# Optimization experiments

Measured on AMD Instinct MI355X. Metric: run time of the kernel, lower is better.

The kernel has to match this reference:

```python
import jax, jax.numpy as jnp
import numpy as np

FRACTION = 0.33  # from attn_type='query_selector_0.33'


def setup_inputs() -> dict:
    key = jax.random.key(0)
    k1, k2, k3, k4 = jax.random.split(key, 4)
    B, L, DIM_VAL, DIM_ATTN = 8, 4096, 64, 64
    scale = 1.0 / np.sqrt(DIM_VAL).astype(np.float32)
    x = jax.random.normal(k1, (B, L, DIM_VAL), dtype=jnp.float32)
    Wq = jax.random.normal(k2, (DIM_VAL, DIM_ATTN), dtype=jnp.float32) * scale
    Wk = jax.random.normal(k3, (DIM_VAL, DIM_ATTN), dtype=jnp.float32) * scale
    Wv = jax.random.normal(k4, (DIM_VAL, DIM_VAL), dtype=jnp.float32) * scale
    return {"x": x, "Wq": Wq, "Wk": Wk, "Wv": Wv}


def reference(x, Wq, Wk, Wv):
    # Projections (bias-free Linears)
    Q = jnp.einsum('bld,de->ble', x, Wq)  # [B, L, Da]
    K = jnp.einsum('bld,de->ble', x, Wk)  # [B, L, Da]
    V = jnp.einsum('bld,de->ble', x, Wv)  # [B, L, Dv]

    B, L_Q, Da = Q.shape
    l_Q = int((1.0 - FRACTION) * L_Q)  # static: shapes known at trace time

    # keys.topk(l_Q, dim=1).values -> per-channel top-l_Q along seq; mean over them
    K_top = jax.lax.top_k(jnp.swapaxes(K, 1, 2), l_Q)[0]  # [B, Da, l_Q]
    K_reduce = K_top.mean(axis=-1)                         # [B, Da]

    # score each query against the reduced key; pick top-l_Q queries
    sqk = jnp.einsum('bd,bld->bl', K_reduce, Q)            # [B, L_Q]
    indices = jax.lax.top_k(sqk, l_Q)[1]                   # [B, l_Q] int32

    # gather sampled queries
    Q_sample = jnp.take_along_axis(Q, indices[:, :, None], axis=1)  # [B, l_Q, Da]

    # dense attention for the sampled queries only
    scores = jnp.einsum('bqd,bkd->bqk', Q_sample, K) / jnp.sqrt(jnp.asarray(Da, Q.dtype))
    attn = jax.nn.softmax(scores, axis=-1)                 # [B, l_Q, L]
    out_sel = jnp.einsum('bqk,bkv->bqv', attn, V)          # [B, l_Q, Dv]

    # mean-filled result, scatter attention outputs to selected rows
    mean_values = V.mean(axis=-2)                          # [B, Dv]
    result = jnp.broadcast_to(mean_values[:, None, :], (B, L_Q, V.shape[-1]))
    result = result.at[jnp.arange(B)[:, None], indices].set(out_sel)
    return result
```

## Files before the change

### kernel.cpp

```cpp
#include <hip/hip_runtime.h>
#include <hip/hip_bf16.h>
#include <math.h>

#define BATCH 8
#define SEQ   4096
#define DIM   64
#define LQ    2744
#define QPB   128
#define NQB   22
#define QPAD  2816
#define KS    8
#define L2E   1.4426950408889634f
#define QSC   0.1803368801111204f

typedef _Float16 half8 __attribute__((ext_vector_type(8)));
typedef short    bs8   __attribute__((ext_vector_type(8)));
typedef float    fx16  __attribute__((ext_vector_type(16)));
typedef unsigned short ushort_t;

union UH { uint4 u4; half8 h; };
union UB { unsigned u[4]; uint4 u4; bs8 s; };

__device__ __forceinline__ unsigned pack_bf16(float a, float b) {
    unsigned ua = __float_as_uint(a), ub = __float_as_uint(b);
    ua += 0x7FFFu + ((ua >> 16) & 1u);
    ub += 0x7FFFu + ((ub >> 16) & 1u);
    return (ua >> 16) | (ub & 0xFFFF0000u);
}

__device__ __forceinline__ unsigned f2sort(float f) {
    unsigned u = __float_as_uint(f);
    return (u & 0x80000000u) ? ~u : (u | 0x80000000u);
}
__device__ __forceinline__ float sort2f(unsigned u) {
    return __uint_as_float((u & 0x80000000u) ? (u & 0x7FFFFFFFu) : ~u);
}

template <int NT>
__device__ void radix_select_4096(const unsigned* u, int k, unsigned* hist,
                                  unsigned* scan, unsigned* res) {
    const int t = threadIdx.x;
    if (t == 0) { res[0] = 0u; res[1] = (unsigned)k; }
    for (int pass = 3; pass >= 0; --pass) {
        const int shift = pass * 8;
        if (t < 256) hist[t] = 0u;
        __syncthreads();
        const unsigned pref  = res[0];
        const unsigned kk    = res[1];
        const unsigned hmask = (pass == 3) ? 0u : (0xFFFFFFFFu << (shift + 8));
        for (int i = t; i < 4096; i += NT) {
            unsigned ui = u[i];
            if ((ui & hmask) == pref) atomicAdd(&hist[(ui >> shift) & 255u], 1u);
        }
        __syncthreads();
        unsigned h = 0u, s = 0u;
        if (t < 256) { h = hist[t]; s = h; scan[t] = s; }
        __syncthreads();
#pragma unroll
        for (int ofs = 1; ofs < 256; ofs <<= 1) {
            unsigned add = (t < 256 && t + ofs < 256) ? scan[t + ofs] : 0u;
            __syncthreads();
            if (t < 256) { s += add; scan[t] = s; }
            __syncthreads();
        }
        if (t < 256 && s >= kk && (s - h) < kk) {
            res[0] = pref | ((unsigned)t << shift);
            res[1] = kk - (s - h);
        }
        __syncthreads();
    }
}

__global__ __launch_bounds__(256) void proj_kernel(
    const float* __restrict__ x,  const float* __restrict__ Wq,
    const float* __restrict__ Wk, const float* __restrict__ Wv,
    float* __restrict__ Q, float* __restrict__ Kt,
    _Float16* __restrict__ Qh, _Float16* __restrict__ Kh,
    ushort_t* __restrict__ Vt, float* __restrict__ pmean) {
    const int rt = blockIdx.x, b = blockIdx.y, t = threadIdx.x;
    __shared__ float4 xs4[64 * 17];
    __shared__ float  red[4][64];
    {
        const float4* xg = (const float4*)(x + ((size_t)b * SEQ + rt * 64) * DIM);
        for (int i = 0; i < 4; ++i) {
            int s = t + 256 * i;
            xs4[(s >> 4) * 17 + (s & 15)] = xg[s];
        }
    }
    __syncthreads();
    const int ch = t & 63, rg = t >> 6;
    float accq[16], acck[16], accv[16];
#pragma unroll
    for (int i = 0; i < 16; ++i) { accq[i] = 0.f; acck[i] = 0.f; accv[i] = 0.f; }
    for (int dc = 0; dc < 4; ++dc) {
        float wq[16], wk[16], wv[16];
#pragma unroll
        for (int dd = 0; dd < 16; ++dd) {
            int d = dc * 16 + dd;
            wq[dd] = Wq[d * 64 + ch]; wk[dd] = Wk[d * 64 + ch]; wv[dd] = Wv[d * 64 + ch];
        }
        for (int r = 0; r < 16; ++r) {
            const int row = rg * 16 + r;
            const float4* xr = &xs4[row * 17 + dc * 4];
            float xv[16];
            float4 a0 = xr[0], a1 = xr[1], a2 = xr[2], a3 = xr[3];
            xv[0]=a0.x; xv[1]=a0.y; xv[2]=a0.z; xv[3]=a0.w;
            xv[4]=a1.x; xv[5]=a1.y; xv[6]=a1.z; xv[7]=a1.w;
            xv[8]=a2.x; xv[9]=a2.y; xv[10]=a2.z; xv[11]=a2.w;
            xv[12]=a3.x; xv[13]=a3.y; xv[14]=a3.z; xv[15]=a3.w;
#pragma unroll
            for (int dd = 0; dd < 16; ++dd) {
                accq[r] = fmaf(xv[dd], wq[dd], accq[r]);
                acck[r] = fmaf(xv[dd], wk[dd], acck[r]);
                accv[r] = fmaf(xv[dd], wv[dd], accv[r]);
            }
        }
    }
    const int rowbase = rt * 64 + rg * 16;
    float sv = 0.f;
#pragma unroll
    for (int r = 0; r < 16; ++r) {
        size_t o = ((size_t)b * SEQ + rowbase + r) * DIM + ch;
        Q[o]  = accq[r];
        Qh[o] = (_Float16)(accq[r] * QSC);
        Kh[o] = (_Float16)acck[r];
        sv += accv[r];
    }
    float4* ktp = (float4*)(Kt + ((size_t)b * 64 + ch) * SEQ + rowbase);
    ktp[0] = make_float4(acck[0], acck[1], acck[2], acck[3]);
    ktp[1] = make_float4(acck[4], acck[5], acck[6], acck[7]);
    ktp[2] = make_float4(acck[8], acck[9], acck[10], acck[11]);
    ktp[3] = make_float4(acck[12], acck[13], acck[14], acck[15]);
    {
        unsigned pk[8];
#pragma unroll
        for (int i = 0; i < 8; ++i) {
            __hip_bfloat162 h2 = __float22bfloat162_rn(make_float2(accv[2*i], accv[2*i+1]));
            union { __hip_bfloat162 h; unsigned u; } cv; cv.h = h2;
            pk[i] = cv.u;
        }
        uint4* vp = (uint4*)(Vt + ((size_t)(b * 64 + ch)) * SEQ + rowbase);
        vp[0] = make_uint4(pk[0], pk[1], pk[4], pk[5]);
        vp[1] = make_uint4(pk[2], pk[3], pk[6], pk[7]);
    }
    red[rg][ch] = sv;
    __syncthreads();
    if (rg == 0)
        pmean[((size_t)b * 64 + ch) * 64 + rt] =
            red[0][ch] + red[1][ch] + red[2][ch] + red[3][ch];
}

__global__ __launch_bounds__(1024) void kmean_kernel(const float* __restrict__ Kt,
                                                     const float* __restrict__ pmean,
                                                     float* __restrict__ Kred,
                                                     float* __restrict__ meanfin) {
    __shared__ unsigned u[4096];
    __shared__ unsigned hist[256];
    __shared__ unsigned scan[256];
    __shared__ unsigned res[2];
    __shared__ float rsum[16];
    const int bc = blockIdx.x, t = threadIdx.x;
    if (t < 64) {
        float v = pmean[(size_t)bc * 64 + t];
        for (int m = 1; m < 64; m <<= 1) v += __shfl_xor(v, m, 64);
        if (t == 0) meanfin[bc] = v * (1.0f / (float)SEQ);
    }
    const float4* c4 = (const float4*)(Kt + (size_t)bc * SEQ);
    if (t < 1024) {
        float4 v = c4[t];
        u[t*4+0] = f2sort(v.x); u[t*4+1] = f2sort(v.y);
        u[t*4+2] = f2sort(v.z); u[t*4+3] = f2sort(v.w);
    }
    __syncthreads();
    radix_select_4096<1024>(u, LQ, hist, scan, res);
    const unsigned Tu = res[0];
    const int krem = (int)res[1];
    float loc = 0.f;
    for (int i = t; i < 4096; i += 1024)
        if (u[i] > Tu) loc += sort2f(u[i]);
    for (int msk = 1; msk < 64; msk <<= 1) loc += __shfl_xor(loc, msk, 64);
    if ((t & 63) == 0) rsum[t >> 6] = loc;
    __syncthreads();
    if (t == 0) {
        float s = (float)krem * sort2f(Tu);
        for (int i = 0; i < 16; ++i) s += rsum[i];
        Kred[bc] = s / (float)LQ;
    }
}

__global__ __launch_bounds__(1024) void select_kernel(const float* __restrict__ Q,
                                                      const float* __restrict__ Kred,
                                                      int* __restrict__ sel,
                                                      int* __restrict__ inv) {
    __shared__ unsigned u[4096];
    __shared__ unsigned hist[256];
    __shared__ unsigned scan[256];
    __shared__ unsigned res[2];
    __shared__ float kr[64];
    __shared__ int eq_idx[256];
    __shared__ int cnts[2];
    const int b = blockIdx.x, t = threadIdx.x;
    if (t < 64) kr[t] = Kred[b * 64 + t];
    if (t < 2) cnts[t] = 0;
    int* invb = inv + (size_t)b * SEQ;
    __syncthreads();
    for (int row = t; row < 4096; row += 1024) {
        const float4* q = (const float4*)(Q + ((size_t)b * SEQ + row) * DIM);
        float s = 0.f;
#pragma unroll
        for (int i = 0; i < 16; ++i) {
            float4 v = q[i];
            s = fmaf(v.x, kr[i*4+0], s); s = fmaf(v.y, kr[i*4+1], s);
            s = fmaf(v.z, kr[i*4+2], s); s = fmaf(v.w, kr[i*4+3], s);
        }
        u[row] = f2sort(s);
        invb[row] = -1;
    }
    __syncthreads();
    radix_select_4096<1024>(u, LQ, hist, scan, res);
    const unsigned Tu = res[0];
    const int krem = (int)res[1];
    int* selb = sel + b * QPAD;
    for (int i = t; i < 4096; i += 1024) {
        unsigned ui = u[i];
        if (ui > Tu) {
            int p = atomicAdd(&cnts[0], 1);
            selb[p] = i;
            invb[i] = p;
        } else if (ui == Tu) {
            int p = atomicAdd(&cnts[1], 1);
            if (p < 256) eq_idx[p] = i;
        }
    }
    __syncthreads();
    if (t == 0) {
        int ng = cnts[0];
        int ne = cnts[1] < 256 ? cnts[1] : 256;
        for (int i = 1; i < ne; ++i) {
            int v = eq_idx[i], j = i - 1;
            while (j >= 0 && eq_idx[j] > v) { eq_idx[j+1] = eq_idx[j]; --j; }
            eq_idx[j+1] = v;
        }
        for (int j = 0; j < krem; ++j) {
            selb[ng + j] = eq_idx[j];
            invb[eq_idx[j]] = ng + j;
        }
    }
    __syncthreads();
    if (t < QPAD - LQ) selb[LQ + t] = selb[LQ - 1];
}

__global__ __launch_bounds__(256, 3) void attn_kernel(
    const ushort_t* __restrict__ Qh, const ushort_t* __restrict__ Kh,
    const ushort_t* __restrict__ Vt, const int* __restrict__ sel,
    float* __restrict__ pl, float* __restrict__ pout) {
    const int qt = blockIdx.x, ks = blockIdx.y, b = blockIdx.z;
    const int t = threadIdx.x, w = t >> 6, lane = t & 63;
    const int col = lane & 31, h = lane >> 5;

    __shared__ ushort_t Ktile[2][32 * 64];
    __shared__ ushort_t Vtile[2][32 * 64];

    half8 qf[4];
    {
        const int q = qt * QPB + w * 32 + col;
        const int row = sel[b * QPAD + q];
        const uint4* qg = (const uint4*)(Qh + ((size_t)b * SEQ + row) * DIM);
#pragma unroll
        for (int m = 0; m < 4; ++m) { UH u; u.u4 = qg[2 * m + h]; qf[m] = u.h; }
    }

    int koff[4], voff[4];
#pragma unroll
    for (int m = 0; m < 4; ++m)
        koff[m] = col * 64 + 8 * ((2 * m + h) ^ (col & 7));
#pragma unroll
    for (int i = 0; i < 4; ++i)
        voff[i] = col * 64 + 8 * ((i * 2 + h) ^ (col & 7));

    fx16 O0, O1;
#pragma unroll
    for (int r = 0; r < 16; ++r) { O0[r] = 0.f; O1[r] = 0.f; }
    float l = 0.f;

    const int srow = t >> 3, sgr = t & 7;
    const int lg = sgr ^ (srow & 7);
    const int vD = lg >> 2, vc = (lg >> 1) & 1, vh = lg & 1;
    const size_t kgbase = ((size_t)b * SEQ + ks * 512 + srow) * DIM + 8 * lg;
    const size_t vgbase = ((size_t)(b * DIM + srow + 32 * vD)) * SEQ
                          + ks * 512 + vc * 16 + vh * 8;

    uint4 kreg = *(const uint4*)(Kh + kgbase);
    uint4 vreg = *(const uint4*)(Vt + vgbase);

    for (int tile = 0; tile < 16; ++tile) {
        const int buf = tile & 1;
        *(uint4*)&Ktile[buf][srow * 64 + sgr * 8] = kreg;
        *(uint4*)&Vtile[buf][srow * 64 + sgr * 8] = vreg;
        __syncthreads();
        if (tile < 15) {
            kreg = *(const uint4*)(Kh + kgbase + (size_t)(tile + 1) * 32 * DIM);
            vreg = *(const uint4*)(Vt + vgbase + (size_t)(tile + 1) * 32);
        }
        fx16 S;
#pragma unroll
        for (int r = 0; r < 16; ++r) S[r] = 0.f;
#pragma unroll
        for (int m = 0; m < 4; ++m) {
            UH kf;
            kf.u4 = *(const uint4*)&Ktile[buf][koff[m]];
            S = __builtin_amdgcn_mfma_f32_32x32x16_f16(kf.h, qf[m], S, 0, 0, 0);
        }
        float p[16];
#pragma unroll
        for (int r = 0; r < 16; ++r) p[r] = __builtin_amdgcn_exp2f(S[r]);
#pragma unroll
        for (int r = 0; r < 16; ++r) l += p[r];
        UB A0, A1;
#pragma unroll
        for (int v = 0; v < 4; ++v) {
            A0.u[v] = pack_bf16(p[2 * v],     p[2 * v + 1]);
            A1.u[v] = pack_bf16(p[8 + 2 * v], p[8 + 2 * v + 1]);
        }
#pragma unroll
        for (int D = 0; D < 2; ++D) {
            fx16& O = D ? O1 : O0;
#pragma unroll
            for (int c = 0; c < 2; ++c) {
                UB vf;
                vf.u4 = *(const uint4*)&Vtile[buf][voff[D * 2 + c]];
                O = __builtin_amdgcn_mfma_f32_32x32x16_bf16(c ? A1.s : A0.s, vf.s, O, 0, 0, 0);
            }
        }
    }

    l += __shfl_xor(l, 32);

    const int qg0 = qt * QPB + w * 32;
    const size_t base = (size_t)b * QPAD + qg0;
#pragma unroll
    for (int D = 0; D < 2; ++D) {
        const fx16& O = D ? O1 : O0;
#pragma unroll
        for (int r = 0; r < 16; ++r) {
            const int q = (r & 3) + 8 * (r >> 2) + 4 * h;
            atomicAdd(&pout[(base + q) * DIM + D * 32 + col], O[r]);
        }
    }
    if (h == 0) atomicAdd(&pl[base + col], l);
}

__global__ __launch_bounds__(256) void comb_kernel(
    const float* __restrict__ pl, const float* __restrict__ pout,
    const int* __restrict__ inv, const float* __restrict__ meanfin,
    float* __restrict__ out) {
    const int idx = blockIdx.x * 256 + threadIdx.x;
    const int b = idx >> 16;
    const int rc = idx & 65535;
    const int row = rc >> 4, c = rc & 15;
    const int p = inv[b * SEQ + row];
    float4 o;
    if (p >= 0) {
        const size_t s0 = (size_t)b * QPAD + p;
        const float invl = 1.0f / pl[s0];
        float4 a = ((const float4*)(pout + s0 * DIM))[c];
        o = make_float4(a.x * invl, a.y * invl, a.z * invl, a.w * invl);
    } else {
        o = make_float4(meanfin[b * 64 + c * 4 + 0], meanfin[b * 64 + c * 4 + 1],
                        meanfin[b * 64 + c * 4 + 2], meanfin[b * 64 + c * 4 + 3]);
    }
    ((float4*)out)[idx] = o;
}

extern "C" void kernel_launch(void* const* d_in, const int* in_sizes, int n_in,
                              void* d_out, int out_size, void* d_ws, size_t ws_size,
                              hipStream_t stream) {
    const float* x  = (const float*)d_in[0];
    const float* Wq = (const float*)d_in[1];
    const float* Wk = (const float*)d_in[2];
    const float* Wv = (const float*)d_in[3];
    float* out = (float*)d_out;
    char* wsb  = (char*)d_ws;

    float*    Q       = (float*)(wsb);
    _Float16* Qh      = (_Float16*)(wsb + 8388608);
    _Float16* Kh      = (_Float16*)(wsb + 12582912);
    ushort_t* Vt      = (ushort_t*)(wsb + 16777216);
    float*    pmean   = (float*)(wsb + 20971520);
    float*    meanfin = (float*)(wsb + 21102592);
    float*    Kred    = (float*)(wsb + 21104640);
    int*      sel     = (int*)(wsb + 21106688);
    int*      inv     = (int*)(wsb + 21196800);
    float*    Kt      = (float*)(wsb + 21327872);
    float*    pout    = (float*)(wsb + 21327872);
    float*    pl      = (float*)(wsb + 21327872 + 5767168);

    proj_kernel  <<<dim3(64, 8),          256,  0, stream>>>(x, Wq, Wk, Wv, Q, Kt,
                                                             Qh, Kh, Vt, pmean);
    kmean_kernel <<<512,                  1024, 0, stream>>>(Kt, pmean, Kred, meanfin);
    select_kernel<<<8,                    1024, 0, stream>>>(Q, Kred, sel, inv);
    hipMemsetAsync(pout, 0, 5767168 + 90112, stream);
    attn_kernel  <<<dim3(NQB, KS, BATCH), 256,  0, stream>>>((const ushort_t*)Qh,
                                                             (const ushort_t*)Kh,
                                                             Vt, sel, pl, pout);
    comb_kernel  <<<2048,                 256,  0, stream>>>(pl, pout, inv, meanfin, out);
}
```

Before: 220.6 us.

## Rework attention tiling, switch P·V to fp16, and speed up radix select

The attention kernel now runs 2 waves of 64 queries each, so every K/V tile loaded into shared memory is reused across two query sub-blocks. V and the softmax probabilities move from bf16 with manual rounding to fp16 using the packed cvt_pkrtz instruction. The radix select now builds its histogram with ballot-based match-any aggregation and replaces the 8-step shared-memory scan with a wave-level shuffle scan. kmean_kernel shrinks to 256 threads per block. These cut shared-memory atomics, barriers and conversion cost, but raise register pressure, and fp16 probabilities lose range compared with bf16.

```diff
diff --git a/kernel.cpp b/kernel.cpp
--- a/kernel.cpp
+++ b/kernel.cpp
@@ -1,5 +1,4 @@
 #include <hip/hip_runtime.h>
-#include <hip/hip_bf16.h>
 #include <math.h>
 
 #define BATCH 8
@@ -10,22 +9,18 @@
 #define NQB   22
 #define QPAD  2816
 #define KS    8
-#define L2E   1.4426950408889634f
 #define QSC   0.1803368801111204f
 
 typedef _Float16 half8 __attribute__((ext_vector_type(8)));
-typedef short    bs8   __attribute__((ext_vector_type(8)));
+typedef __fp16   fp16x2 __attribute__((ext_vector_type(2)));
 typedef float    fx16  __attribute__((ext_vector_type(16)));
 typedef unsigned short ushort_t;
 
-union UH { uint4 u4; half8 h; };
-union UB { unsigned u[4]; uint4 u4; bs8 s; };
-
-__device__ __forceinline__ unsigned pack_bf16(float a, float b) {
-    unsigned ua = __float_as_uint(a), ub = __float_as_uint(b);
-    ua += 0x7FFFu + ((ua >> 16) & 1u);
-    ub += 0x7FFFu + ((ub >> 16) & 1u);
-    return (ua >> 16) | (ub & 0xFFFF0000u);
+union UHF { unsigned u[4]; uint4 u4; half8 h; };
+
+__device__ __forceinline__ unsigned pack_f16(float a, float b) {
+    fp16x2 r = __builtin_amdgcn_cvt_pkrtz(a, b);
+    union { fp16x2 h; unsigned u; } cv; cv.h = r; return cv.u;
 }
 
 __device__ __forceinline__ unsigned f2sort(float f) {
@@ -38,8 +33,9 @@
 
 template <int NT>
 __device__ void radix_select_4096(const unsigned* u, int k, unsigned* hist,
-                                  unsigned* scan, unsigned* res) {
+                                  unsigned* wtot, unsigned* res) {
     const int t = threadIdx.x;
+    const int lane = t & 63, wv = t >> 6;
     if (t == 0) { res[0] = 0u; res[1] = (unsigned)k; }
     for (int pass = 3; pass >= 0; --pass) {
         const int shift = pass * 8;
@@ -49,23 +45,38 @@
         const unsigned kk    = res[1];
         const unsigned hmask = (pass == 3) ? 0u : (0xFFFFFFFFu << (shift + 8));
         for (int i = t; i < 4096; i += NT) {
-            unsigned ui = u[i];
-            if ((ui & hmask) == pref) atomicAdd(&hist[(ui >> shift) & 255u], 1u);
+            const unsigned ui = u[i];
+            const bool part = (ui & hmask) == pref;
+            const unsigned bin = (ui >> shift) & 255u;
+            unsigned long long m = __ballot(part);
+#pragma unroll
+            for (int j = 0; j < 8; ++j) {
+                unsigned long long bj = __ballot(part && ((bin >> j) & 1u));
+                m &= ((bin >> j) & 1u) ? bj : ~bj;
+            }
+            if (part && (1ull << lane) == (m & (0ull - m)))
+                atomicAdd(&hist[bin], (unsigned)__popcll(m));
         }
         __syncthreads();
         unsigned h = 0u, s = 0u;
-        if (t < 256) { h = hist[t]; s = h; scan[t] = s; }
+        if (t < 256) {
+            h = hist[t]; s = h;
+#pragma unroll
+            for (int ofs = 1; ofs < 64; ofs <<= 1) {
+                unsigned o = __shfl_down(s, ofs, 64);
+                if (lane + ofs < 64) s += o;
+            }
+            if (lane == 0) wtot[wv] = s;
+        }
         __syncthreads();
-#pragma unroll
-        for (int ofs = 1; ofs < 256; ofs <<= 1) {
-            unsigned add = (t < 256 && t + ofs < 256) ? scan[t + ofs] : 0u;
-            __syncthreads();
-            if (t < 256) { s += add; scan[t] = s; }
-            __syncthreads();
-        }
-        if (t < 256 && s >= kk && (s - h) < kk) {
-            res[0] = pref | ((unsigned)t << shift);
-            res[1] = kk - (s - h);
+        if (t < 256) {
+            unsigned add = 0u;
+            for (int j = wv + 1; j < 4; ++j) add += wtot[j];
+            s += add;
+            if (s >= kk && (s - h) < kk) {
+                res[0] = pref | ((unsigned)t << shift);
+                res[1] = kk - (s - h);
+            }
         }
         __syncthreads();
     }
@@ -100,8 +111,7 @@
             wq[dd] = Wq[d * 64 + ch]; wk[dd] = Wk[d * 64 + ch]; wv[dd] = Wv[d * 64 + ch];
         }
         for (int r = 0; r < 16; ++r) {
-            const int row = rg * 16 + r;
-            const float4* xr = &xs4[row * 17 + dc * 4];
+            const float4* xr = &xs4[(rg * 16 + r) * 17 + dc * 4];
             float xv[16];
             float4 a0 = xr[0], a1 = xr[1], a2 = xr[2], a3 = xr[3];
             xv[0]=a0.x; xv[1]=a0.y; xv[2]=a0.z; xv[3]=a0.w;
@@ -134,11 +144,7 @@
     {
         unsigned pk[8];
 #pragma unroll
-        for (int i = 0; i < 8; ++i) {
-            __hip_bfloat162 h2 = __float22bfloat162_rn(make_float2(accv[2*i], accv[2*i+1]));
-            union { __hip_bfloat162 h; unsigned u; } cv; cv.h = h2;
-            pk[i] = cv.u;
-        }
+        for (int i = 0; i < 8; ++i) pk[i] = pack_f16(accv[2*i], accv[2*i+1]);
         uint4* vp = (uint4*)(Vt + ((size_t)(b * 64 + ch)) * SEQ + rowbase);
         vp[0] = make_uint4(pk[0], pk[1], pk[4], pk[5]);
         vp[1] = make_uint4(pk[2], pk[3], pk[6], pk[7]);
@@ -150,15 +156,15 @@
             red[0][ch] + red[1][ch] + red[2][ch] + red[3][ch];
 }
 
-__global__ __launch_bounds__(1024) void kmean_kernel(const float* __restrict__ Kt,
-                                                     const float* __restrict__ pmean,
-                                                     float* __restrict__ Kred,
-                                                     float* __restrict__ meanfin) {
+__global__ __launch_bounds__(256) void kmean_kernel(const float* __restrict__ Kt,
+                                                    const float* __restrict__ pmean,
+                                                    float* __restrict__ Kred,
+                                                    float* __restrict__ meanfin) {
     __shared__ unsigned u[4096];
     __shared__ unsigned hist[256];
-    __shared__ unsigned scan[256];
+    __shared__ unsigned wtot[4];
     __shared__ unsigned res[2];
-    __shared__ float rsum[16];
+    __shared__ float rsum[4];
     const int bc = blockIdx.x, t = threadIdx.x;
     if (t < 64) {
         float v = pmean[(size_t)bc * 64 + t];
@@ -166,24 +172,23 @@
         if (t == 0) meanfin[bc] = v * (1.0f / (float)SEQ);
     }
     const float4* c4 = (const float4*)(Kt + (size_t)bc * SEQ);
-    if (t < 1024) {
-        float4 v = c4[t];
-        u[t*4+0] = f2sort(v.x); u[t*4+1] = f2sort(v.y);
-        u[t*4+2] = f2sort(v.z); u[t*4+3] = f2sort(v.w);
-    }
-    __syncthreads();
-    radix_select_4096<1024>(u, LQ, hist, scan, res);
+    for (int i = t; i < 1024; i += 256) {
+        float4 v = c4[i];
+        u[i*4+0] = f2sort(v.x); u[i*4+1] = f2sort(v.y);
+        u[i*4+2] = f2sort(v.z); u[i*4+3] = f2sort(v.w);
+    }
+    __syncthreads();
+    radix_select_4096<256>(u, LQ, hist, wtot, res);
     const unsigned Tu = res[0];
     const int krem = (int)res[1];
     float loc = 0.f;
-    for (int i = t; i < 4096; i += 1024)
+    for (int i = t; i < 4096; i += 256)
         if (u[i] > Tu) loc += sort2f(u[i]);
     for (int msk = 1; msk < 64; msk <<= 1) loc += __shfl_xor(loc, msk, 64);
     if ((t & 63) == 0) rsum[t >> 6] = loc;
     __syncthreads();
     if (t == 0) {
-        float s = (float)krem * sort2f(Tu);
-        for (int i = 0; i < 16; ++i) s += rsum[i];
+        float s = rsum[0] + rsum[1] + rsum[2] + rsum[3] + (float)krem * sort2f(Tu);
         Kred[bc] = s / (float)LQ;
     }
 }
@@ -194,7 +199,7 @@
                                                       int* __restrict__ inv) {
     __shared__ unsigned u[4096];
     __shared__ unsigned hist[256];
-    __shared__ unsigned scan[256];
+    __shared__ unsigned wtot[4];
     __shared__ unsigned res[2];
     __shared__ float kr[64];
     __shared__ int eq_idx[256];
@@ -217,7 +222,7 @@
         invb[row] = -1;
     }
     __syncthreads();
-    radix_select_4096<1024>(u, LQ, hist, scan, res);
+    radix_select_4096<1024>(u, LQ, hist, wtot, res);
     const unsigned Tu = res[0];
     const int krem = (int)res[1];
     int* selb = sel + b * QPAD;
@@ -250,7 +255,7 @@
     if (t < QPAD - LQ) selb[LQ + t] = selb[LQ - 1];
 }
 
-__global__ __launch_bounds__(256, 3) void attn_kernel(
+__global__ __launch_bounds__(128, 2) void attn_kernel(
     const ushort_t* __restrict__ Qh, const ushort_t* __restrict__ Kh,
     const ushort_t* __restrict__ Vt, const int* __restrict__ sel,
     float* __restrict__ pl, float* __restrict__ pout) {
@@ -261,13 +266,19 @@
     __shared__ ushort_t Ktile[2][32 * 64];
     __shared__ ushort_t Vtile[2][32 * 64];
 
-    half8 qf[4];
+    half8 qfa[4], qfb[4];
+    const int qbase = qt * QPB + w * 64;
     {
-        const int q = qt * QPB + w * 32 + col;
-        const int row = sel[b * QPAD + q];
-        const uint4* qg = (const uint4*)(Qh + ((size_t)b * SEQ + row) * DIM);
-#pragma unroll
-        for (int m = 0; m < 4; ++m) { UH u; u.u4 = qg[2 * m + h]; qf[m] = u.h; }
+        const int rowa = sel[b * QPAD + qbase + col];
+        const int rowb = sel[b * QPAD + qbase + 32 + col];
+        const uint4* qga = (const uint4*)(Qh + ((size_t)b * SEQ + rowa) * DIM);
+        const uint4* qgb = (const uint4*)(Qh + ((size_t)b * SEQ + rowb) * DIM);
+#pragma unroll
+        for (int m = 0; m < 4; ++m) {
+            UHF ua, ub;
+            ua.u4 = qga[2 * m + h]; qfa[m] = ua.h;
+            ub.u4 = qgb[2 * m + h]; qfb[m] = ub.h;
+        }
     }
 
     int koff[4], voff[4];
@@ -278,76 +289,95 @@
     for (int i = 0; i < 4; ++i)
         voff[i] = col * 64 + 8 * ((i * 2 + h) ^ (col & 7));
 
-    fx16 O0, O1;
-#pragma unroll
-    for (int r = 0; r < 16; ++r) { O0[r] = 0.f; O1[r] = 0.f; }
-    float l = 0.f;
+    fx16 Oa0, Oa1, Ob0, Ob1;
+#pragma unroll
+    for (int r = 0; r < 16; ++r) { Oa0[r]=0.f; Oa1[r]=0.f; Ob0[r]=0.f; Ob1[r]=0.f; }
+    float la = 0.f, lb = 0.f;
 
     const int srow = t >> 3, sgr = t & 7;
     const int lg = sgr ^ (srow & 7);
     const int vD = lg >> 2, vc = (lg >> 1) & 1, vh = lg & 1;
-    const size_t kgbase = ((size_t)b * SEQ + ks * 512 + srow) * DIM + 8 * lg;
-    const size_t vgbase = ((size_t)(b * DIM + srow + 32 * vD)) * SEQ
+    const ushort_t* kp0 = Kh + ((size_t)b * SEQ + ks * 512 + srow) * DIM + 8 * lg;
+    const ushort_t* kp1 = kp0 + 16 * DIM;
+    const ushort_t* vp0 = Vt + ((size_t)(b * DIM + srow + 32 * vD)) * SEQ
                           + ks * 512 + vc * 16 + vh * 8;
-
-    uint4 kreg = *(const uint4*)(Kh + kgbase);
-    uint4 vreg = *(const uint4*)(Vt + vgbase);
+    const ushort_t* vp1 = vp0 + 16 * SEQ;
+
+    uint4 kr0 = *(const uint4*)kp0, kr1 = *(const uint4*)kp1;
+    uint4 vr0 = *(const uint4*)vp0, vr1 = *(const uint4*)vp1;
 
     for (int tile = 0; tile < 16; ++tile) {
         const int buf = tile & 1;
-        *(uint4*)&Ktile[buf][srow * 64 + sgr * 8] = kreg;
-        *(uint4*)&Vtile[buf][srow * 64 + sgr * 8] = vreg;
+        *(uint4*)&Ktile[buf][srow * 64 + sgr * 8]        = kr0;
+        *(uint4*)&Ktile[buf][(srow + 16) * 64 + sgr * 8] = kr1;
+        *(uint4*)&Vtile[buf][srow * 64 + sgr * 8]        = vr0;
+        *(uint4*)&Vtile[buf][(srow + 16) * 64 + sgr * 8] = vr1;
         __syncthreads();
         if (tile < 15) {
-            kreg = *(const uint4*)(Kh + kgbase + (size_t)(tile + 1) * 32 * DIM);
-            vreg = *(const uint4*)(Vt + vgbase + (size_t)(tile + 1) * 32);
-        }
-        fx16 S;
-#pragma unroll
-        for (int r = 0; r < 16; ++r) S[r] = 0.f;
+            kp0 += 32 * DIM; kp1 += 32 * DIM; vp0 += 32; vp1 += 32;
+            kr0 = *(const uint4*)kp0; kr1 = *(const uint4*)kp1;
+            vr0 = *(const uint4*)vp0; vr1 = *(const uint4*)vp1;
+        }
+        fx16 Sa, Sb;
+#pragma unroll
+        for (int r = 0; r < 16; ++r) { Sa[r] = 0.f; Sb[r] = 0.f; }
+        UHF kf[4];
+#pragma unroll
+        for (int m = 0; m < 4; ++m)
+            kf[m].u4 = *(const uint4*)&Ktile[buf][koff[m]];
 #pragma unroll
         for (int m = 0; m < 4; ++m) {
-            UH kf;
-            kf.u4 = *(const uint4*)&Ktile[buf][koff[m]];
-            S = __builtin_amdgcn_mfma_f32_32x32x16_f16(kf.h, qf[m], S, 0, 0, 0);
-        }
-        float p[16];
-#pragma unroll
-        for (int r = 0; r < 16; ++r) p[r] = __builtin_amdgcn_exp2f(S[r]);
-#pragma unroll
-        for (int r = 0; r < 16; ++r) l += p[r];
-        UB A0, A1;
+            Sa = __builtin_amdgcn_mfma_f32_32x32x16_f16(kf[m].h, qfa[m], Sa, 0, 0, 0);
+            Sb = __builtin_amdgcn_mfma_f32_32x32x16_f16(kf[m].h, qfb[m], Sb, 0, 0, 0);
+        }
+        UHF Aa0, Aa1, Ab0, Ab1;
 #pragma unroll
         for (int v = 0; v < 4; ++v) {
-            A0.u[v] = pack_bf16(p[2 * v],     p[2 * v + 1]);
-            A1.u[v] = pack_bf16(p[8 + 2 * v], p[8 + 2 * v + 1]);
-        }
-#pragma unroll
-        for (int D = 0; D < 2; ++D) {
-            fx16& O = D ? O1 : O0;
-#pragma unroll
-            for (int c = 0; c < 2; ++c) {
-                UB vf;
-                vf.u4 = *(const uint4*)&Vtile[buf][voff[D * 2 + c]];
-                O = __builtin_amdgcn_mfma_f32_32x32x16_bf16(c ? A1.s : A0.s, vf.s, O, 0, 0, 0);
-            }
-        }
-    }
-
-    l += __shfl_xor(l, 32);
-
-    const int qg0 = qt * QPB + w * 32;
-    const size_t base = (size_t)b * QPAD + qg0;
-#pragma unroll
-    for (int D = 0; D < 2; ++D) {
-        const fx16& O = D ? O1 : O0;
-#pragma unroll
-        for (int r = 0; r < 16; ++r) {
-            const int q = (r & 3) + 8 * (r >> 2) + 4 * h;
-            atomicAdd(&pout[(base + q) * DIM + D * 32 + col], O[r]);
-        }
-    }
-    if (h == 0) atomicAdd(&pl[base + col], l);
+            float a0 = __builtin_amdgcn_exp2f(Sa[2*v]);
+            float a1 = __builtin_amdgcn_exp2f(Sa[2*v+1]);
+            float a2 = __builtin_amdgcn_exp2f(Sa[8+2*v]);
+            float a3 = __builtin_amdgcn_exp2f(Sa[8+2*v+1]);
+            la += (a0 + a1) + (a2 + a3);
+            Aa0.u[v] = pack_f16(a0, a1);
+            Aa1.u[v] = pack_f16(a2, a3);
+            float b0 = __builtin_amdgcn_exp2f(Sb[2*v]);
+            float b1 = __builtin_amdgcn_exp2f(Sb[2*v+1]);
+            float b2 = __builtin_amdgcn_exp2f(Sb[8+2*v]);
+            float b3 = __builtin_amdgcn_exp2f(Sb[8+2*v+1]);
+            lb += (b0 + b1) + (b2 + b3);
+            Ab0.u[v] = pack_f16(b0, b1);
+            Ab1.u[v] = pack_f16(b2, b3);
+        }
+        UHF vf[4];
+#pragma unroll
+        for (int i = 0; i < 4; ++i)
+            vf[i].u4 = *(const uint4*)&Vtile[buf][voff[i]];
+        Oa0 = __builtin_amdgcn_mfma_f32_32x32x16_f16(Aa0.h, vf[0].h, Oa0, 0, 0, 0);
+        Ob0 = __builtin_amdgcn_mfma_f32_32x32x16_f16(Ab0.h, vf[0].h, Ob0, 0, 0, 0);
+        Oa0 = __builtin_amdgcn_mfma_f32_32x32x16_f16(Aa1.h, vf[1].h, Oa0, 0, 0, 0);
+        Ob0 = __builtin_amdgcn_mfma_f32_32x32x16_f16(Ab1.h, vf[1].h, Ob0, 0, 0, 0);
+        Oa1 = __builtin_amdgcn_mfma_f32_32x32x16_f16(Aa0.h, vf[2].h, Oa1, 0, 0, 0);
+        Ob1 = __builtin_amdgcn_mfma_f32_32x32x16_f16(Ab0.h, vf[2].h, Ob1, 0, 0, 0);
+        Oa1 = __builtin_amdgcn_mfma_f32_32x32x16_f16(Aa1.h, vf[3].h, Oa1, 0, 0, 0);
+        Ob1 = __builtin_amdgcn_mfma_f32_32x32x16_f16(Ab1.h, vf[3].h, Ob1, 0, 0, 0);
+    }
+
+    la += __shfl_xor(la, 32);
+    lb += __shfl_xor(lb, 32);
+
+    const size_t base = (size_t)b * QPAD + qbase;
+#pragma unroll
+    for (int r = 0; r < 16; ++r) {
+        const int q = (r & 3) + 8 * (r >> 2) + 4 * h;
+        atomicAdd(&pout[(base + q) * DIM + col],           Oa0[r]);
+        atomicAdd(&pout[(base + q) * DIM + 32 + col],      Oa1[r]);
+        atomicAdd(&pout[(base + 32 + q) * DIM + col],      Ob0[r]);
+        atomicAdd(&pout[(base + 32 + q) * DIM + 32 + col], Ob1[r]);
+    }
+    if (h == 0) {
+        atomicAdd(&pl[base + col], la);
+        atomicAdd(&pl[base + 32 + col], lb);
+    }
 }
 
 __global__ __launch_bounds__(256) void comb_kernel(
@@ -397,10 +427,10 @@
 
     proj_kernel  <<<dim3(64, 8),          256,  0, stream>>>(x, Wq, Wk, Wv, Q, Kt,
                                                              Qh, Kh, Vt, pmean);
-    kmean_kernel <<<512,                  1024, 0, stream>>>(Kt, pmean, Kred, meanfin);
+    kmean_kernel <<<512,                  256,  0, stream>>>(Kt, pmean, Kred, meanfin);
     select_kernel<<<8,                    1024, 0, stream>>>(Q, Kred, sel, inv);
-    hipMemsetAsync(pout, 0, 5767168 + 90112, stream);
-    attn_kernel  <<<dim3(NQB, KS, BATCH), 256,  0, stream>>>((const ushort_t*)Qh,
+    (void)hipMemsetAsync(pout, 0, 5767168 + 90112, stream);
+    attn_kernel  <<<dim3(NQB, KS, BATCH), 128,  0, stream>>>((const ushort_t*)Qh,
                                                              (const ushort_t*)Kh,
                                                              Vt, sel, pl, pout);
     comb_kernel  <<<2048,                 256,  0, stream>>>(pl, pout, inv, meanfin, out);
```

New measurement: 247.0 us. +12.0%, slower.
